# Kernel tuning notes

Hardware: AMD Instinct MI355X
Metric: run time of the kernel (lower is better)

Reference implementation:

```python
import jax, jax.numpy as jnp
import numpy as np

NEG_SLOPE = 0.2  # PyG GATv2Conv default negative_slope


def gatv2_conv(x, src, dst, n_nodes, Wl, bl, Wr, br, att, bias):
    """One GATv2Conv layer (concat=True, add_self_loops already applied).
    x: [N, Fin]; src/dst: [E]; Wl/Wr: [Fin, H*C]; att: [H, C]; bias: [H*C].
    Returns [N, H*C]."""
    H, C = att.shape
    xl = (x @ Wl + bl).reshape(n_nodes, H, C)  # source transform (x_j)
    xr = (x @ Wr + br).reshape(n_nodes, H, C)  # target transform (x_i)
    # per-edge GATv2 score: a^T LeakyReLU(xl_j + xr_i)
    e = jax.nn.leaky_relu(xl[src] + xr[dst], NEG_SLOPE)      # [E, H, C]
    score = jnp.einsum('ehc,hc->eh', e, att)                 # [E, H]
    # segment softmax over incoming edges of each destination node
    m = jax.lax.stop_gradient(
        jax.ops.segment_max(score, dst, num_segments=n_nodes))  # [N, H]
    p = jnp.exp(score - m[dst])                               # [E, H]
    s = jax.ops.segment_sum(p, dst, num_segments=n_nodes)     # [N, H]
    alpha = p / s[dst]                                        # [E, H]
    out = jax.ops.segment_sum(alpha[:, :, None] * xl[src], dst,
                              num_segments=n_nodes)           # [N, H, C]
    return out.reshape(n_nodes, H * C) + bias


def setup_inputs() -> dict:
    key = jax.random.key(0)
    ks = jax.random.split(key, 16)
    N, Fin, H, C = 20000, 64, 4, 64
    E = 500000
    Fmid = H * C  # 256

    def glorot(k, shape):
        fan_in, fan_out = shape[0], shape[-1]
        lim = np.sqrt(6.0 / (fan_in + fan_out))
        return jax.random.uniform(k, shape, jnp.float32, -lim, lim)

    return {
        'x': jax.random.normal(ks[0], (N, Fin), jnp.float32),
        'edge_index': jax.random.randint(ks[1], (2, E), 0, N, jnp.int64),
        # layer 1: in=64, out=64, heads=4
        'Wl1': glorot(ks[2], (Fin, H * C)),
        'bl1': jnp.zeros((H * C,), jnp.float32),
        'Wr1': glorot(ks[3], (Fin, H * C)),
        'br1': jnp.zeros((H * C,), jnp.float32),
        'att1': glorot(ks[4], (H, C)),
        'bias1': jnp.zeros((H * C,), jnp.float32),
        # layer 2: in=256, out=64, heads=4
        'Wl2': glorot(ks[5], (Fmid, H * C)),
        'bl2': jnp.zeros((H * C,), jnp.float32),
        'Wr2': glorot(ks[6], (Fmid, H * C)),
        'br2': jnp.zeros((H * C,), jnp.float32),
        'att2': glorot(ks[7], (H, C)),
        'bias2': jnp.zeros((H * C,), jnp.float32),
    }


def reference(x, edge_index, Wl1, bl1, Wr1, br1, att1, bias1,
              Wl2, bl2, Wr2, br2, att2, bias2):
    N = x.shape[0]
    # PyG add_self_loops=True default
    loop = jnp.arange(N, dtype=edge_index.dtype)
    src = jnp.concatenate([edge_index[0], loop])
    dst = jnp.concatenate([edge_index[1], loop])

    h = gatv2_conv(x, src, dst, N, Wl1, bl1, Wr1, br1, att1, bias1)
    h = jax.nn.elu(h)
    h = gatv2_conv(h, src, dst, N, Wl2, bl2, Wr2, br2, att2, bias2)
    return (h, jax.nn.log_softmax(h, axis=1))
```

## Files before the change

kernel.cpp:

```cpp
#include <hip/hip_runtime.h>
#include <math.h>

#define NEG_SLOPE 0.2f

typedef unsigned short ushort_t;
typedef __attribute__((ext_vector_type(8))) short short8;
typedef __attribute__((ext_vector_type(4))) float float4v;
typedef _Float16 half2v __attribute__((ext_vector_type(2)));

#if defined(__has_builtin)
#if __has_builtin(__builtin_amdgcn_fdot2)
#define HAS_FDOT2 1
#endif
#if __has_builtin(__builtin_amdgcn_update_dpp)
#define HAS_DPP 1
#endif
#endif

__device__ __forceinline__ ushort_t f2bf(float f) {
    unsigned u = __float_as_uint(f);
    return (ushort_t)((u + 0x7fffu + ((u >> 16) & 1u)) >> 16);
}
__device__ __forceinline__ unsigned pack2bf(float lo, float hi) {
    return ((unsigned)f2bf(hi) << 16) | (unsigned)f2bf(lo);
}

#if HAS_DPP
template <int CTRL>
__device__ __forceinline__ float dppf(float x) {
    return __uint_as_float((unsigned)__builtin_amdgcn_update_dpp(
        0, (int)__float_as_uint(x), CTRL, 0xF, 0xF, true));
}
#endif

__global__ void hist_kernel(const int* __restrict__ dst, int* __restrict__ deg, int E) {
    int i = blockIdx.x * 256 + threadIdx.x;
    if (i < E) atomicAdd(&deg[dst[i]], 1);
}

__global__ void partial_kernel(const int* __restrict__ deg, int* __restrict__ partial, int n) {
    const int t = threadIdx.x;
    const int i = blockIdx.x * 256 + t;
    int v = (i < n) ? deg[i] : 0;
#pragma unroll
    for (int off = 32; off > 0; off >>= 1) v += __shfl_xor(v, off, 64);
    __shared__ int ws[4];
    if ((t & 63) == 0) ws[t >> 6] = v;
    __syncthreads();
    if (t == 0) partial[blockIdx.x] = ws[0] + ws[1] + ws[2] + ws[3];
}

__global__ void scan_kernel(const int* __restrict__ in, int* __restrict__ out, int n) {
    __shared__ int sm[1024];
    __shared__ int carry_s;
    const int t = threadIdx.x;
    if (t == 0) { carry_s = 0; out[0] = 0; }
    __syncthreads();
    for (int base = 0; base < n; base += 1024) {
        int v = (base + t < n) ? in[base + t] : 0;
        sm[t] = v;
        __syncthreads();
        for (int off = 1; off < 1024; off <<= 1) {
            int u = (t >= off) ? sm[t - off] : 0;
            __syncthreads();
            sm[t] += u;
            __syncthreads();
        }
        if (base + t < n) out[base + t + 1] = carry_s + sm[t];
        __syncthreads();
        if (t == 0) carry_s += sm[1023];
        __syncthreads();
    }
}

__global__ void scan_block_kernel(const int* __restrict__ deg, const int* __restrict__ blk_off,
                                  int* __restrict__ row_ptr, int n) {
    const int t = threadIdx.x;
    const int i = blockIdx.x * 256 + t;
    const int lane = t & 63, w = t >> 6;
    int x = (i < n) ? deg[i] : 0;
#pragma unroll
    for (int off = 1; off < 64; off <<= 1) {
        int u = __shfl_up(x, off, 64);
        if (lane >= off) x += u;
    }
    __shared__ int ws[4];
    if (lane == 63) ws[w] = x;
    __syncthreads();
    int add = blk_off[blockIdx.x];
#pragma unroll
    for (int j = 0; j < 4; ++j)
        if (j < w) add += ws[j];
    if (i < n) row_ptr[i + 1] = add + x;
    if (i == 0) row_ptr[0] = 0;
}

__global__ void scatter_kernel(const int* __restrict__ src, const int* __restrict__ dst,
                               const int* __restrict__ row_ptr, int* __restrict__ cursor,
                               int* __restrict__ csr_src, int E) {
    int i = blockIdx.x * 256 + threadIdx.x;
    if (i < E) {
        int d = dst[i];
        int pos = row_ptr[d] + atomicAdd(&cursor[d], 1);
        csr_src[pos] = src[i];
    }
}

__global__ void wt_all_kernel(const float* __restrict__ W1l, const float* __restrict__ W1r,
                              const float* __restrict__ W2l, const float* __restrict__ W2r,
                              ushort_t* __restrict__ T1l, ushort_t* __restrict__ T1r,
                              ushort_t* __restrict__ T2l, ushort_t* __restrict__ T2r) {
    const int b = blockIdx.x;
    const float* W;
    ushort_t* T;
    int K, idx;
    if (b < 64)       { W = W1l; T = T1l; K = 64;  idx = b * 256 + threadIdx.x; }
    else if (b < 128) { W = W1r; T = T1r; K = 64;  idx = (b - 64) * 256 + threadIdx.x; }
    else if (b < 384) { W = W2l; T = T2l; K = 256; idx = (b - 128) * 256 + threadIdx.x; }
    else              { W = W2r; T = T2r; K = 256; idx = (b - 384) * 256 + threadIdx.x; }
    const int k = idx >> 8, c = idx & 255;
    T[(size_t)c * K + k] = f2bf(W[idx]);
}

template <int K, bool A_FP32>
__global__ __launch_bounds__(256) void gemm_dual_kernel(const void* __restrict__ Av,
                                                        const ushort_t* __restrict__ BTl,
                                                        const ushort_t* __restrict__ BTr,
                                                        const float* __restrict__ bl,
                                                        const float* __restrict__ br,
                                                        _Float16* __restrict__ outl,
                                                        _Float16* __restrict__ outr, int M) {
    __shared__ ushort_t As[2][64][40];
    __shared__ ushort_t Bs[2][2][128][40];
    const int t = threadIdx.x;
    const int row0 = blockIdx.x * 64, col0 = blockIdx.y * 128;
    const int wid = t >> 6, lane = t & 63;
    const int wr = wid >> 1, wc = wid & 1;
    const int frow = lane & 15, fk = (lane >> 4) * 8;
    const int arow = t >> 2, ak8 = (t & 3) * 8;
    const int srow = t >> 1, sks = (t & 1) * 16;

    float4v acc[2][2][4];
#pragma unroll
    for (int m = 0; m < 2; ++m)
#pragma unroll
        for (int i = 0; i < 2; ++i)
#pragma unroll
            for (int j = 0; j < 4; ++j) acc[m][i][j] = (float4v){0.f, 0.f, 0.f, 0.f};

    auto stage = [&](int buf, int k0) {
        uint4 va = make_uint4(0, 0, 0, 0);
        if (row0 + arow < M) {
            if (A_FP32) {
                const float* Xf = (const float*)Av + (size_t)(row0 + arow) * K + k0 + ak8;
                float4 x0 = *(const float4*)(Xf + 0);
                float4 x1 = *(const float4*)(Xf + 4);
                va = make_uint4(pack2bf(x0.x, x0.y), pack2bf(x0.z, x0.w),
                                pack2bf(x1.x, x1.y), pack2bf(x1.z, x1.w));
            } else {
                va = *(const uint4*)((const ushort_t*)Av + (size_t)(row0 + arow) * K + k0 + ak8);
            }
        }
        *(uint4*)&As[buf][arow][ak8] = va;
        const ushort_t* Bp = BTl + (size_t)(col0 + srow) * K + k0 + sks;
        *(uint4*)&Bs[buf][0][srow][sks + 0] = *(const uint4*)(Bp + 0);
        *(uint4*)&Bs[buf][0][srow][sks + 8] = *(const uint4*)(Bp + 8);
        const ushort_t* Bq = BTr + (size_t)(col0 + srow) * K + k0 + sks;
        *(uint4*)&Bs[buf][1][srow][sks + 0] = *(const uint4*)(Bq + 0);
        *(uint4*)&Bs[buf][1][srow][sks + 8] = *(const uint4*)(Bq + 8);
    };

    stage(0, 0);
    __syncthreads();
    int cur = 0;
    for (int k0 = 0; k0 < K; k0 += 32) {
        if (k0 + 32 < K) stage(cur ^ 1, k0 + 32);
        short8 af[2], bf[2][4];
#pragma unroll
        for (int mi = 0; mi < 2; ++mi)
            af[mi] = *(const short8*)&As[cur][wr * 32 + mi * 16 + frow][fk];
#pragma unroll
        for (int m = 0; m < 2; ++m)
#pragma unroll
            for (int ni = 0; ni < 4; ++ni)
                bf[m][ni] = *(const short8*)&Bs[cur][m][wc * 64 + ni * 16 + frow][fk];
#pragma unroll
        for (int m = 0; m < 2; ++m)
#pragma unroll
            for (int mi = 0; mi < 2; ++mi)
#pragma unroll
                for (int ni = 0; ni < 4; ++ni)
                    acc[m][mi][ni] = __builtin_amdgcn_mfma_f32_16x16x32_bf16(
                        af[mi], bf[m][ni], acc[m][mi][ni], 0, 0, 0);
        __syncthreads();
        cur ^= 1;
    }

    const int crow = (lane >> 4) * 4;
#pragma unroll
    for (int ni = 0; ni < 4; ++ni) {
        const int col = col0 + wc * 64 + ni * 16 + frow;
        const float bvl = bl[col], bvr = br[col];
#pragma unroll
        for (int mi = 0; mi < 2; ++mi) {
#pragma unroll
            for (int r = 0; r < 4; ++r) {
                const int row = row0 + wr * 32 + mi * 16 + crow + r;
                if (row < M) {
                    outl[(size_t)row * 256 + col] = (_Float16)(acc[0][mi][ni][r] + bvl);
                    outr[(size_t)row * 256 + col] = (_Float16)(acc[1][mi][ni][r] + bvr);
                }
            }
        }
    }
}

__global__ __launch_bounds__(128) void gat_fused_kernel(const int* __restrict__ csr_src,
                                                        const int* __restrict__ row_ptr,
                                                        const _Float16* __restrict__ xl,
                                                        const _Float16* __restrict__ xr,
                                                        const float* __restrict__ att,
                                                        const float* __restrict__ bias,
                                                        ushort_t* __restrict__ out_b,
                                                        float* __restrict__ out,
                                                        float* __restrict__ out_ls,
                                                        int n_nodes, int apply_elu) {
    const int wv = threadIdx.x >> 6;
    const int d = blockIdx.x * 2 + wv;
    if (d >= n_nodes) return;
    const int lane = threadIdx.x & 63;
    const int e = lane >> 5;
    const int g = lane & 31;
    const int off = g * 8;

    union U8 { uint4 u; _Float16 h[8]; half2v h2[4]; };
    U8 xru;
    xru.u = *(const uint4*)(xr + (size_t)d * 256 + off);
    float avf[8];
    *(float4*)&avf[0] = *(const float4*)(att + off);
    *(float4*)&avf[4] = *(const float4*)(att + off + 4);
#if HAS_FDOT2
    half2v xr2[4], a06[4], a04[4];
#pragma unroll
    for (int i = 0; i < 4; ++i) {
        xr2[i] = xru.h2[i];
        a06[i] = (half2v){(_Float16)(0.6f * avf[2 * i]), (_Float16)(0.6f * avf[2 * i + 1])};
        a04[i] = (half2v){(_Float16)(0.4f * avf[2 * i]), (_Float16)(0.4f * avf[2 * i + 1])};
    }
#else
    float xrf[8];
#pragma unroll
    for (int i = 0; i < 8; ++i) xrf[i] = (float)xru.h[i];
#endif
    const int e0 = row_ptr[d];
    const int deg = row_ptr[d + 1] - e0;
    const int cnt = deg + 1;
    const int nchunk = (cnt + 1) >> 1;
    float m = -INFINITY, s_loc = 0.f;
    float acc8[8] = {0.f, 0.f, 0.f, 0.f, 0.f, 0.f, 0.f, 0.f};

    U8 gc;
    {
        const int j = e;
        const int sn = (j < deg) ? csr_src[e0 + j] : d;
        gc.u = *(const uint4*)(xl + (size_t)sn * 256 + off);
    }
    int sn_nxt = d;
    if (nchunk > 1) {
        const int j = 2 + e;
        sn_nxt = (j < deg) ? csr_src[e0 + j] : d;
    }

    for (int c = 0; c < nchunk; ++c) {
        const int base = c << 1;
        int sn_n2 = d;
        if (c + 2 < nchunk) {
            const int j = base + 4 + e;
            sn_n2 = (j < deg) ? csr_src[e0 + j] : d;
        }
        U8 gn;
        gn.u = make_uint4(0, 0, 0, 0);
        if (c + 1 < nchunk) gn.u = *(const uint4*)(xl + (size_t)sn_nxt * 256 + off);

        const int j = base + e;
        float sc = 0.f;
#if HAS_FDOT2
#pragma unroll
        for (int i = 0; i < 4; ++i) {
            half2v v = gc.h2[i] + xr2[i];
            unsigned vb = __builtin_bit_cast(unsigned, v);
            half2v va = __builtin_bit_cast(half2v, vb & 0x7fff7fffu);
            sc = __builtin_amdgcn_fdot2(v, a06[i], sc, false);
            sc = __builtin_amdgcn_fdot2(va, a04[i], sc, false);
        }
#else
#pragma unroll
        for (int i = 0; i < 8; ++i) {
            float v = (float)gc.h[i] + xrf[i];
            v = fmaxf(v, NEG_SLOPE * v);
            sc = fmaf(v, avf[i], sc);
        }
#endif
#if HAS_DPP
        sc += dppf<0xB1>(sc);
        sc += dppf<0x4E>(sc);
#else
        sc += __shfl_xor(sc, 1, 64);
        sc += __shfl_xor(sc, 2, 64);
#endif
        sc += __shfl_xor(sc, 4, 64);
        sc = (j < cnt) ? sc : -INFINITY;
        float mx = fmaxf(sc, __shfl_xor(sc, 32, 64));
        if (mx > m + 8.f) {
            const float g2f = __expf(m - mx);
            s_loc *= g2f;
#pragma unroll
            for (int i = 0; i < 8; ++i) acc8[i] *= g2f;
            m = mx;
        }
        const float p = __expf(sc - m);
        s_loc += p;
#pragma unroll
        for (int i = 0; i < 8; ++i)
            acc8[i] = fmaf(p, (float)gc.h[i], acc8[i]);

        gc = gn;
        sn_nxt = sn_n2;
    }

    float s_tot = s_loc + __shfl_xor(s_loc, 32, 64);
#pragma unroll
    for (int i = 0; i < 8; ++i) acc8[i] += __shfl_xor(acc8[i], 32, 64);
    const float inv_s = 1.f / s_tot;
    float o8[8];
    const float* bp = bias + off;
#pragma unroll
    for (int i = 0; i < 8; ++i) o8[i] = acc8[i] * inv_s + bp[i];

    if (apply_elu) {
#pragma unroll
        for (int i = 0; i < 8; ++i) o8[i] = o8[i] > 0.f ? o8[i] : (__expf(o8[i]) - 1.f);
        if (e == 0) {
            uint4 u;
            u.x = pack2bf(o8[0], o8[1]);
            u.y = pack2bf(o8[2], o8[3]);
            u.z = pack2bf(o8[4], o8[5]);
            u.w = pack2bf(o8[6], o8[7]);
            *(uint4*)(out_b + (size_t)d * 256 + off) = u;
        }
    } else {
        if (e == 0) {
            float* op = out + (size_t)d * 256 + off;
            *(float4*)op       = make_float4(o8[0], o8[1], o8[2], o8[3]);
            *(float4*)(op + 4) = make_float4(o8[4], o8[5], o8[6], o8[7]);
        }
        float mx = o8[0];
#pragma unroll
        for (int i = 1; i < 8; ++i) mx = fmaxf(mx, o8[i]);
        mx = fmaxf(mx, __shfl_xor(mx, 1, 64));
        mx = fmaxf(mx, __shfl_xor(mx, 2, 64));
        mx = fmaxf(mx, __shfl_xor(mx, 4, 64));
        mx = fmaxf(mx, __shfl_xor(mx, 8, 64));
        mx = fmaxf(mx, __shfl_xor(mx, 16, 64));
        float se = 0.f;
#pragma unroll
        for (int i = 0; i < 8; ++i) se += __expf(o8[i] - mx);
        se += __shfl_xor(se, 1, 64);
        se += __shfl_xor(se, 2, 64);
        se += __shfl_xor(se, 4, 64);
        se += __shfl_xor(se, 8, 64);
        se += __shfl_xor(se, 16, 64);
        const float lg = mx + __logf(se);
        if (e == 0) {
            float* lp = out_ls + (size_t)d * 256 + off;
            *(float4*)lp       = make_float4(o8[0] - lg, o8[1] - lg, o8[2] - lg, o8[3] - lg);
            *(float4*)(lp + 4) = make_float4(o8[4] - lg, o8[5] - lg, o8[6] - lg, o8[7] - lg);
        }
    }
}

extern "C" void kernel_launch(void* const* d_in, const int* in_sizes, int n_in,
                              void* d_out, int out_size, void* d_ws, size_t ws_size,
                              hipStream_t stream) {
    const float* x     = (const float*)d_in[0];
    const int*   edge  = (const int*)d_in[1];
    const float* Wl1   = (const float*)d_in[2];
    const float* bl1   = (const float*)d_in[3];
    const float* Wr1   = (const float*)d_in[4];
    const float* br1   = (const float*)d_in[5];
    const float* att1  = (const float*)d_in[6];
    const float* bias1 = (const float*)d_in[7];
    const float* Wl2   = (const float*)d_in[8];
    const float* bl2   = (const float*)d_in[9];
    const float* Wr2   = (const float*)d_in[10];
    const float* br2   = (const float*)d_in[11];
    const float* att2  = (const float*)d_in[12];
    const float* bias2 = (const float*)d_in[13];

    const int N = in_sizes[0] / 64;
    const int E = in_sizes[1] / 2;
    const int* srcI = edge;
    const int* dstI = edge + E;

    const size_t NM = (size_t)N * 256;
    _Float16*  XR   = (_Float16*)d_ws;
    ushort_t*  XB   = (ushort_t*)(XR + NM);
    _Float16*  XL   = (_Float16*)(XB + NM);
    ushort_t*  WT1l = (ushort_t*)(XL + NM);
    ushort_t*  WT1r = WT1l + 256 * 64;
    ushort_t*  WT2l = WT1r + 256 * 64;
    ushort_t*  WT2r = WT2l + 256 * 256;
    int* deg     = (int*)(WT2r + 256 * 256);
    int* cursor  = deg + N;
    int* row_ptr = cursor + N;
    int* partial = row_ptr + N + 1;
    int* blk_off = partial + ((N + 255) / 256);
    int* csr_src = blk_off + ((N + 255) / 256) + 1;

    const int nb = (N + 255) / 256;
    const int e_grid = (E + 255) / 256;
    const dim3 gemm_grid((N + 63) / 64, 2);
    const int gat_grid = (N + 1) / 2;

    wt_all_kernel<<<640, 256, 0, stream>>>(Wl1, Wr1, Wl2, Wr2, WT1l, WT1r, WT2l, WT2r);

    hipMemsetAsync(deg, 0, (size_t)(2 * N) * sizeof(int), stream);
    hist_kernel<<<e_grid, 256, 0, stream>>>(dstI, deg, E);
    partial_kernel<<<nb, 256, 0, stream>>>(deg, partial, N);
    scan_kernel<<<1, 1024, 0, stream>>>(partial, blk_off, nb);
    scan_block_kernel<<<nb, 256, 0, stream>>>(deg, blk_off, row_ptr, N);
    scatter_kernel<<<e_grid, 256, 0, stream>>>(srcI, dstI, row_ptr, cursor, csr_src, E);

    gemm_dual_kernel<64, true><<<gemm_grid, 256, 0, stream>>>(x, WT1l, WT1r, bl1, br1,
                                                              XL, XR, N);
    gat_fused_kernel<<<gat_grid, 128, 0, stream>>>(csr_src, row_ptr, XL, XR, att1, bias1,
                                                   XB, nullptr, nullptr, N, 1);

    gemm_dual_kernel<256, false><<<gemm_grid, 256, 0, stream>>>(XB, WT2l, WT2r, bl2, br2,
                                                                XL, XR, N);
    float* h2 = (float*)d_out;
    gat_fused_kernel<<<gat_grid, 128, 0, stream>>>(csr_src, row_ptr, XL, XR, att2, bias2,
                                                   nullptr, h2, h2 + NM, N, 0);
}
```

Measured before the change: 200.6 us.

## Process four edges per wave step with 16 lanes per edge row

Remaps the fused attention/aggregation kernel so each wave handles four edges per iteration, with 16 lanes each covering 16 channels, instead of two edges with 32 lanes of 8 channels. Each head's 64 channels now span 4 lanes, so the head-score reduction needs one fewer shuffle, and the number of serial online-softmax steps per node is halved. Cost: more registers per lane (16 accumulators and two gather buffers), an extra cross-group max and a final reduce over four edge groups. Low-degree nodes also waste more lanes on padded edges.

```diff
diff --git a/kernel.cpp b/kernel.cpp
--- a/kernel.cpp
+++ b/kernel.cpp
@@ -229,76 +229,102 @@
     const int d = blockIdx.x * 2 + wv;
     if (d >= n_nodes) return;
     const int lane = threadIdx.x & 63;
-    const int e = lane >> 5;
-    const int g = lane & 31;
-    const int off = g * 8;
+    const int e = lane >> 4;
+    const int g = lane & 15;
+    const int off = g * 16;
 
     union U8 { uint4 u; _Float16 h[8]; half2v h2[4]; };
-    U8 xru;
-    xru.u = *(const uint4*)(xr + (size_t)d * 256 + off);
-    float avf[8];
-    *(float4*)&avf[0] = *(const float4*)(att + off);
-    *(float4*)&avf[4] = *(const float4*)(att + off + 4);
+    U8 xr0, xr1;
+    xr0.u = *(const uint4*)(xr + (size_t)d * 256 + off);
+    xr1.u = *(const uint4*)(xr + (size_t)d * 256 + off + 8);
+    float avf[16];
+#pragma unroll
+    for (int q = 0; q < 4; ++q)
+        *(float4*)&avf[q * 4] = *(const float4*)(att + off + q * 4);
 #if HAS_FDOT2
-    half2v xr2[4], a06[4], a04[4];
-#pragma unroll
-    for (int i = 0; i < 4; ++i) {
-        xr2[i] = xru.h2[i];
+    half2v xr2[8], a06[8], a04[8];
+#pragma unroll
+    for (int i = 0; i < 4; ++i) { xr2[i] = xr0.h2[i]; xr2[4 + i] = xr1.h2[i]; }
+#pragma unroll
+    for (int i = 0; i < 8; ++i) {
         a06[i] = (half2v){(_Float16)(0.6f * avf[2 * i]), (_Float16)(0.6f * avf[2 * i + 1])};
         a04[i] = (half2v){(_Float16)(0.4f * avf[2 * i]), (_Float16)(0.4f * avf[2 * i + 1])};
     }
 #else
-    float xrf[8];
-#pragma unroll
-    for (int i = 0; i < 8; ++i) xrf[i] = (float)xru.h[i];
+    float xrf[16];
+#pragma unroll
+    for (int i = 0; i < 8; ++i) { xrf[i] = (float)xr0.h[i]; xrf[8 + i] = (float)xr1.h[i]; }
 #endif
     const int e0 = row_ptr[d];
     const int deg = row_ptr[d + 1] - e0;
     const int cnt = deg + 1;
-    const int nchunk = (cnt + 1) >> 1;
+    const int nchunk = (cnt + 3) >> 2;
     float m = -INFINITY, s_loc = 0.f;
-    float acc8[8] = {0.f, 0.f, 0.f, 0.f, 0.f, 0.f, 0.f, 0.f};
-
-    U8 gc;
+    float acc[16];
+#pragma unroll
+    for (int i = 0; i < 16; ++i) acc[i] = 0.f;
+
+    U8 gc0, gc1;
     {
         const int j = e;
         const int sn = (j < deg) ? csr_src[e0 + j] : d;
-        gc.u = *(const uint4*)(xl + (size_t)sn * 256 + off);
+        const _Float16* p = xl + (size_t)sn * 256 + off;
+        gc0.u = *(const uint4*)p;
+        gc1.u = *(const uint4*)(p + 8);
     }
     int sn_nxt = d;
     if (nchunk > 1) {
-        const int j = 2 + e;
+        const int j = 4 + e;
         sn_nxt = (j < deg) ? csr_src[e0 + j] : d;
     }
 
     for (int c = 0; c < nchunk; ++c) {
-        const int base = c << 1;
+        const int base = c << 2;
         int sn_n2 = d;
         if (c + 2 < nchunk) {
-            const int j = base + 4 + e;
+            const int j = base + 8 + e;
             sn_n2 = (j < deg) ? csr_src[e0 + j] : d;
         }
-        U8 gn;
-        gn.u = make_uint4(0, 0, 0, 0);
-        if (c + 1 < nchunk) gn.u = *(const uint4*)(xl + (size_t)sn_nxt * 256 + off);
+        U8 gn0, gn1;
+        gn0.u = make_uint4(0, 0, 0, 0);
+        gn1.u = make_uint4(0, 0, 0, 0);
+        if (c + 1 < nchunk) {
+            const _Float16* p = xl + (size_t)sn_nxt * 256 + off;
+            gn0.u = *(const uint4*)p;
+            gn1.u = *(const uint4*)(p + 8);
+        }
 
         const int j = base + e;
         float sc = 0.f;
 #if HAS_FDOT2
 #pragma unroll
         for (int i = 0; i < 4; ++i) {
-            half2v v = gc.h2[i] + xr2[i];
+            half2v v = gc0.h2[i] + xr2[i];
             unsigned vb = __builtin_bit_cast(unsigned, v);
             half2v va = __builtin_bit_cast(half2v, vb & 0x7fff7fffu);
             sc = __builtin_amdgcn_fdot2(v, a06[i], sc, false);
             sc = __builtin_amdgcn_fdot2(va, a04[i], sc, false);
         }
+#pragma unroll
+        for (int i = 0; i < 4; ++i) {
+            half2v v = gc1.h2[i] + xr2[4 + i];
+            unsigned vb = __builtin_bit_cast(unsigned, v);
+            half2v va = __builtin_bit_cast(half2v, vb & 0x7fff7fffu);
+            sc = __builtin_amdgcn_fdot2(v, a06[4 + i], sc, false);
+            sc = __builtin_amdgcn_fdot2(va, a04[4 + i], sc, false);
+        }
 #else
 #pragma unroll
         for (int i = 0; i < 8; ++i) {
-            float v = (float)gc.h[i] + xrf[i];
+            float v = (float)gc0.h[i] + xrf[i];
             v = fmaxf(v, NEG_SLOPE * v);
             sc = fmaf(v, avf[i], sc);
+        }
+#pragma unroll
+        for (int i = 0; i < 8; ++i) {
+            float v = (float)gc1.h[i] + xrf[8 + i];
+            v = fmaxf(v, NEG_SLOPE * v);
+            sc = fmaf(v, avf[8 + i], sc);
         }
 #endif
 #if HAS_DPP
@@ -308,73 +334,89 @@
         sc += __shfl_xor(sc, 1, 64);
         sc += __shfl_xor(sc, 2, 64);
 #endif
-        sc += __shfl_xor(sc, 4, 64);
         sc = (j < cnt) ? sc : -INFINITY;
-        float mx = fmaxf(sc, __shfl_xor(sc, 32, 64));
+        float mx = fmaxf(sc, __shfl_xor(sc, 16, 64));
+        mx = fmaxf(mx, __shfl_xor(mx, 32, 64));
         if (mx > m + 8.f) {
             const float g2f = __expf(m - mx);
             s_loc *= g2f;
 #pragma unroll
-            for (int i = 0; i < 8; ++i) acc8[i] *= g2f;
+            for (int i = 0; i < 16; ++i) acc[i] *= g2f;
             m = mx;
         }
         const float p = __expf(sc - m);
         s_loc += p;
 #pragma unroll
         for (int i = 0; i < 8; ++i)
-            acc8[i] = fmaf(p, (float)gc.h[i], acc8[i]);
-
-        gc = gn;
+            acc[i] = fmaf(p, (float)gc0.h[i], acc[i]);
+#pragma unroll
+        for (int i = 0; i < 8; ++i)
+            acc[8 + i] = fmaf(p, (float)gc1.h[i], acc[8 + i]);
+
+        gc0 = gn0;
+        gc1 = gn1;
         sn_nxt = sn_n2;
     }
 
-    float s_tot = s_loc + __shfl_xor(s_loc, 32, 64);
-#pragma unroll
-    for (int i = 0; i < 8; ++i) acc8[i] += __shfl_xor(acc8[i], 32, 64);
+    float s_tot = s_loc + __shfl_xor(s_loc, 16, 64);
+    s_tot += __shfl_xor(s_tot, 32, 64);
+#pragma unroll
+    for (int i = 0; i < 16; ++i) {
+        acc[i] += __shfl_xor(acc[i], 16, 64);
+        acc[i] += __shfl_xor(acc[i], 32, 64);
+    }
     const float inv_s = 1.f / s_tot;
-    float o8[8];
+    float o[16];
     const float* bp = bias + off;
 #pragma unroll
-    for (int i = 0; i < 8; ++i) o8[i] = acc8[i] * inv_s + bp[i];
+    for (int i = 0; i < 16; ++i) o[i] = acc[i] * inv_s + bp[i];
 
     if (apply_elu) {
 #pragma unroll
-        for (int i = 0; i < 8; ++i) o8[i] = o8[i] > 0.f ? o8[i] : (__expf(o8[i]) - 1.f);
+        for (int i = 0; i < 16; ++i) o[i] = o[i] > 0.f ? o[i] : (__expf(o[i]) - 1.f);
         if (e == 0) {
-            uint4 u;
-            u.x = pack2bf(o8[0], o8[1]);
-            u.y = pack2bf(o8[2], o8[3]);
-            u.z = pack2bf(o8[4], o8[5]);
-            u.w = pack2bf(o8[6], o8[7]);
-            *(uint4*)(out_b + (size_t)d * 256 + off) = u;
+            uint4 u0, u1;
+            u0.x = pack2bf(o[0], o[1]);
+            u0.y = pack2bf(o[2], o[3]);
+            u0.z = pack2bf(o[4], o[5]);
+            u0.w = pack2bf(o[6], o[7]);
+            u1.x = pack2bf(o[8], o[9]);
+            u1.y = pack2bf(o[10], o[11]);
+            u1.z = pack2bf(o[12], o[13]);
+            u1.w = pack2bf(o[14], o[15]);
+            ushort_t* op = out_b + (size_t)d * 256 + off;
+            *(uint4*)op       = u0;
+            *(uint4*)(op + 8) = u1;
         }
     } else {
         if (e == 0) {
             float* op = out + (size_t)d * 256 + off;
-            *(float4*)op       = make_float4(o8[0], o8[1], o8[2], o8[3]);
-            *(float4*)(op + 4) = make_float4(o8[4], o8[5], o8[6], o8[7]);
-        }
-        float mx = o8[0];
-#pragma unroll
-        for (int i = 1; i < 8; ++i) mx = fmaxf(mx, o8[i]);
+#pragma unroll
+            for (int q = 0; q < 4; ++q)
+                *(float4*)(op + q * 4) = make_float4(o[q * 4], o[q * 4 + 1],
+                                                     o[q * 4 + 2], o[q * 4 + 3]);
+        }
+        float mx = o[0];
+#pragma unroll
+        for (int i = 1; i < 16; ++i) mx = fmaxf(mx, o[i]);
         mx = fmaxf(mx, __shfl_xor(mx, 1, 64));
         mx = fmaxf(mx, __shfl_xor(mx, 2, 64));
         mx = fmaxf(mx, __shfl_xor(mx, 4, 64));
         mx = fmaxf(mx, __shfl_xor(mx, 8, 64));
-        mx = fmaxf(mx, __shfl_xor(mx, 16, 64));
         float se = 0.f;
 #pragma unroll
-        for (int i = 0; i < 8; ++i) se += __expf(o8[i] - mx);
+        for (int i = 0; i < 16; ++i) se += __expf(o[i] - mx);
         se += __shfl_xor(se, 1, 64);
         se += __shfl_xor(se, 2, 64);
         se += __shfl_xor(se, 4, 64);
         se += __shfl_xor(se, 8, 64);
-        se += __shfl_xor(se, 16, 64);
         const float lg = mx + __logf(se);
         if (e == 0) {
             float* lp = out_ls + (size_t)d * 256 + off;
-            *(float4*)lp       = make_float4(o8[0] - lg, o8[1] - lg, o8[2] - lg, o8[3] - lg);
-            *(float4*)(lp + 4) = make_float4(o8[4] - lg, o8[5] - lg, o8[6] - lg, o8[7] - lg);
+#pragma unroll
+            for (int q = 0; q < 4; ++q)
+                *(float4*)(lp + q * 4) = make_float4(o[q * 4] - lg, o[q * 4 + 1] - lg,
+                                                     o[q * 4 + 2] - lg, o[q * 4 + 3] - lg);
         }
     }
 }
```

After: 197.0 us. About the same (-1.8%).

## Switch to head-major feature layout with per-head GAT kernels and separate log-softmax

Applied to the files above, without the earlier changes.

The GEMM now writes xl/xr in a head-major layout ([H][N][64]). Aggregation runs as four per-head kernel launches, so each gathered source row is 128 bytes and the per-head working set (about 2.5MB fp16) fits in cache. A wave now processes 8 edges per chunk, one 64-channel head each, instead of 2 edges across all 256 channels. Log-softmax moves into its own kernel, and the CSR scatter reuses the per-edge rank returned by the histogram atomics instead of a second atomic pass. The cost is extra launches, an extra read and write of the output for log-softmax, and wider shuffle reductions.

```diff
diff --git a/kernel.cpp b/kernel.cpp
--- a/kernel.cpp
+++ b/kernel.cpp
@@ -33,9 +33,10 @@
 }
 #endif
 
-__global__ void hist_kernel(const int* __restrict__ dst, int* __restrict__ deg, int E) {
+__global__ void hist_kernel(const int* __restrict__ dst, int* __restrict__ deg,
+                            int* __restrict__ rank, int E) {
     int i = blockIdx.x * 256 + threadIdx.x;
-    if (i < E) atomicAdd(&deg[dst[i]], 1);
+    if (i < E) rank[i] = atomicAdd(&deg[dst[i]], 1);
 }
 
 __global__ void partial_kernel(const int* __restrict__ deg, int* __restrict__ partial, int n) {
@@ -96,13 +97,12 @@
 }
 
 __global__ void scatter_kernel(const int* __restrict__ src, const int* __restrict__ dst,
-                               const int* __restrict__ row_ptr, int* __restrict__ cursor,
+                               const int* __restrict__ row_ptr, const int* __restrict__ rank,
                                int* __restrict__ csr_src, int E) {
     int i = blockIdx.x * 256 + threadIdx.x;
     if (i < E) {
         int d = dst[i];
-        int pos = row_ptr[d] + atomicAdd(&cursor[d], 1);
-        csr_src[pos] = src[i];
+        csr_src[row_ptr[d] + rank[i]] = src[i];
     }
 }
 
@@ -201,44 +201,44 @@
     for (int ni = 0; ni < 4; ++ni) {
         const int col = col0 + wc * 64 + ni * 16 + frow;
         const float bvl = bl[col], bvr = br[col];
+        const size_t hbase = (size_t)(col >> 6) * M * 64 + (col & 63);
 #pragma unroll
         for (int mi = 0; mi < 2; ++mi) {
 #pragma unroll
             for (int r = 0; r < 4; ++r) {
                 const int row = row0 + wr * 32 + mi * 16 + crow + r;
                 if (row < M) {
-                    outl[(size_t)row * 256 + col] = (_Float16)(acc[0][mi][ni][r] + bvl);
-                    outr[(size_t)row * 256 + col] = (_Float16)(acc[1][mi][ni][r] + bvr);
+                    outl[hbase + (size_t)row * 64] = (_Float16)(acc[0][mi][ni][r] + bvl);
+                    outr[hbase + (size_t)row * 64] = (_Float16)(acc[1][mi][ni][r] + bvr);
                 }
             }
         }
     }
 }
 
-__global__ __launch_bounds__(128) void gat_fused_kernel(const int* __restrict__ csr_src,
-                                                        const int* __restrict__ row_ptr,
-                                                        const _Float16* __restrict__ xl,
-                                                        const _Float16* __restrict__ xr,
-                                                        const float* __restrict__ att,
-                                                        const float* __restrict__ bias,
-                                                        ushort_t* __restrict__ out_b,
-                                                        float* __restrict__ out,
-                                                        float* __restrict__ out_ls,
-                                                        int n_nodes, int apply_elu) {
+__global__ __launch_bounds__(128) void gat_head_kernel(const int* __restrict__ csr_src,
+                                                       const int* __restrict__ row_ptr,
+                                                       const _Float16* __restrict__ xlh,
+                                                       const _Float16* __restrict__ xrh,
+                                                       const float* __restrict__ atth,
+                                                       const float* __restrict__ biash,
+                                                       ushort_t* __restrict__ outb,
+                                                       float* __restrict__ outf,
+                                                       int n_nodes, int apply_elu) {
     const int wv = threadIdx.x >> 6;
     const int d = blockIdx.x * 2 + wv;
     if (d >= n_nodes) return;
     const int lane = threadIdx.x & 63;
-    const int e = lane >> 5;
-    const int g = lane & 31;
+    const int e = lane >> 3;
+    const int g = lane & 7;
     const int off = g * 8;
 
     union U8 { uint4 u; _Float16 h[8]; half2v h2[4]; };
     U8 xru;
-    xru.u = *(const uint4*)(xr + (size_t)d * 256 + off);
+    xru.u = *(const uint4*)(xrh + (size_t)d * 64 + off);
     float avf[8];
-    *(float4*)&avf[0] = *(const float4*)(att + off);
-    *(float4*)&avf[4] = *(const float4*)(att + off + 4);
+    *(float4*)&avf[0] = *(const float4*)(atth + off);
+    *(float4*)&avf[4] = *(const float4*)(atth + off + 4);
 #if HAS_FDOT2
     half2v xr2[4], a06[4], a04[4];
 #pragma unroll
@@ -255,32 +255,32 @@
     const int e0 = row_ptr[d];
     const int deg = row_ptr[d + 1] - e0;
     const int cnt = deg + 1;
-    const int nchunk = (cnt + 1) >> 1;
+    const int nchunk = (cnt + 7) >> 3;
     float m = -INFINITY, s_loc = 0.f;
-    float acc8[8] = {0.f, 0.f, 0.f, 0.f, 0.f, 0.f, 0.f, 0.f};
+    float acc[8] = {0.f, 0.f, 0.f, 0.f, 0.f, 0.f, 0.f, 0.f};
 
     U8 gc;
     {
         const int j = e;
         const int sn = (j < deg) ? csr_src[e0 + j] : d;
-        gc.u = *(const uint4*)(xl + (size_t)sn * 256 + off);
+        gc.u = *(const uint4*)(xlh + (size_t)sn * 64 + off);
     }
     int sn_nxt = d;
     if (nchunk > 1) {
-        const int j = 2 + e;
+        const int j = 8 + e;
         sn_nxt = (j < deg) ? csr_src[e0 + j] : d;
     }
 
     for (int c = 0; c < nchunk; ++c) {
-        const int base = c << 1;
+        const int base = c << 3;
         int sn_n2 = d;
         if (c + 2 < nchunk) {
-            const int j = base + 4 + e;
+            const int j = base + 16 + e;
             sn_n2 = (j < deg) ? csr_src[e0 + j] : d;
         }
         U8 gn;
         gn.u = make_uint4(0, 0, 0, 0);
-        if (c + 1 < nchunk) gn.u = *(const uint4*)(xl + (size_t)sn_nxt * 256 + off);
+        if (c + 1 < nchunk) gn.u = *(const uint4*)(xlh + (size_t)sn_nxt * 64 + off);
 
         const int j = base + e;
         float sc = 0.f;
@@ -310,73 +310,80 @@
 #endif
         sc += __shfl_xor(sc, 4, 64);
         sc = (j < cnt) ? sc : -INFINITY;
-        float mx = fmaxf(sc, __shfl_xor(sc, 32, 64));
+        float mx = fmaxf(sc, __shfl_xor(sc, 8, 64));
+        mx = fmaxf(mx, __shfl_xor(mx, 16, 64));
+        mx = fmaxf(mx, __shfl_xor(mx, 32, 64));
         if (mx > m + 8.f) {
             const float g2f = __expf(m - mx);
             s_loc *= g2f;
 #pragma unroll
-            for (int i = 0; i < 8; ++i) acc8[i] *= g2f;
+            for (int i = 0; i < 8; ++i) acc[i] *= g2f;
             m = mx;
         }
         const float p = __expf(sc - m);
         s_loc += p;
 #pragma unroll
         for (int i = 0; i < 8; ++i)
-            acc8[i] = fmaf(p, (float)gc.h[i], acc8[i]);
+            acc[i] = fmaf(p, (float)gc.h[i], acc[i]);
 
         gc = gn;
         sn_nxt = sn_n2;
     }
 
-    float s_tot = s_loc + __shfl_xor(s_loc, 32, 64);
-#pragma unroll
-    for (int i = 0; i < 8; ++i) acc8[i] += __shfl_xor(acc8[i], 32, 64);
+    float s_tot = s_loc + __shfl_xor(s_loc, 8, 64);
+    s_tot += __shfl_xor(s_tot, 16, 64);
+    s_tot += __shfl_xor(s_tot, 32, 64);
+#pragma unroll
+    for (int i = 0; i < 8; ++i) {
+        acc[i] += __shfl_xor(acc[i], 8, 64);
+        acc[i] += __shfl_xor(acc[i], 16, 64);
+        acc[i] += __shfl_xor(acc[i], 32, 64);
+    }
     const float inv_s = 1.f / s_tot;
-    float o8[8];
-    const float* bp = bias + off;
-#pragma unroll
-    for (int i = 0; i < 8; ++i) o8[i] = acc8[i] * inv_s + bp[i];
+    float o[8];
+#pragma unroll
+    for (int i = 0; i < 8; ++i) o[i] = acc[i] * inv_s + biash[off + i];
 
     if (apply_elu) {
 #pragma unroll
-        for (int i = 0; i < 8; ++i) o8[i] = o8[i] > 0.f ? o8[i] : (__expf(o8[i]) - 1.f);
+        for (int i = 0; i < 8; ++i) o[i] = o[i] > 0.f ? o[i] : (__expf(o[i]) - 1.f);
         if (e == 0) {
             uint4 u;
-            u.x = pack2bf(o8[0], o8[1]);
-            u.y = pack2bf(o8[2], o8[3]);
-            u.z = pack2bf(o8[4], o8[5]);
-            u.w = pack2bf(o8[6], o8[7]);
-            *(uint4*)(out_b + (size_t)d * 256 + off) = u;
+            u.x = pack2bf(o[0], o[1]);
+            u.y = pack2bf(o[2], o[3]);
+            u.z = pack2bf(o[4], o[5]);
+            u.w = pack2bf(o[6], o[7]);
+            *(uint4*)(outb + (size_t)d * 256 + off) = u;
         }
     } else {
         if (e == 0) {
-            float* op = out + (size_t)d * 256 + off;
-            *(float4*)op       = make_float4(o8[0], o8[1], o8[2], o8[3]);
-            *(float4*)(op + 4) = make_float4(o8[4], o8[5], o8[6], o8[7]);
-        }
-        float mx = o8[0];
-#pragma unroll
-        for (int i = 1; i < 8; ++i) mx = fmaxf(mx, o8[i]);
-        mx = fmaxf(mx, __shfl_xor(mx, 1, 64));
-        mx = fmaxf(mx, __shfl_xor(mx, 2, 64));
-        mx = fmaxf(mx, __shfl_xor(mx, 4, 64));
-        mx = fmaxf(mx, __shfl_xor(mx, 8, 64));
-        mx = fmaxf(mx, __shfl_xor(mx, 16, 64));
-        float se = 0.f;
-#pragma unroll
-        for (int i = 0; i < 8; ++i) se += __expf(o8[i] - mx);
-        se += __shfl_xor(se, 1, 64);
-        se += __shfl_xor(se, 2, 64);
-        se += __shfl_xor(se, 4, 64);
-        se += __shfl_xor(se, 8, 64);
-        se += __shfl_xor(se, 16, 64);
-        const float lg = mx + __logf(se);
-        if (e == 0) {
-            float* lp = out_ls + (size_t)d * 256 + off;
-            *(float4*)lp       = make_float4(o8[0] - lg, o8[1] - lg, o8[2] - lg, o8[3] - lg);
-            *(float4*)(lp + 4) = make_float4(o8[4] - lg, o8[5] - lg, o8[6] - lg, o8[7] - lg);
-        }
-    }
+            float* op = outf + (size_t)d * 256 + off;
+            *(float4*)op       = make_float4(o[0], o[1], o[2], o[3]);
+            *(float4*)(op + 4) = make_float4(o[4], o[5], o[6], o[7]);
+        }
+    }
+}
+
+__global__ void log_softmax_kernel(const float* __restrict__ in,
+                                   float* __restrict__ out, int n_nodes) {
+    __shared__ float red[8];
+    const int n = blockIdx.x;
+    const int t = threadIdx.x;
+    const int wave = t >> 6, lane = t & 63;
+    const float v = in[(size_t)n * 256 + t];
+    float mx = v;
+#pragma unroll
+    for (int off = 32; off > 0; off >>= 1) mx = fmaxf(mx, __shfl_xor(mx, off, 64));
+    if (lane == 0) red[wave] = mx;
+    __syncthreads();
+    const float m4 = fmaxf(fmaxf(red[0], red[1]), fmaxf(red[2], red[3]));
+    float sum = __expf(v - m4);
+#pragma unroll
+    for (int off = 32; off > 0; off >>= 1) sum += __shfl_xor(sum, off, 64);
+    if (lane == 0) red[4 + wave] = sum;
+    __syncthreads();
+    const float s4 = (red[4] + red[5]) + (red[6] + red[7]);
+    out[(size_t)n * 256 + t] = v - m4 - __logf(s4);
 }
 
 extern "C" void kernel_launch(void* const* d_in, const int* in_sizes, int n_in,
@@ -403,6 +410,7 @@
     const int* dstI = edge + E;
 
     const size_t NM = (size_t)N * 256;
+    const size_t NH = (size_t)N * 64;
     _Float16*  XR   = (_Float16*)d_ws;
     ushort_t*  XB   = (ushort_t*)(XR + NM);
     _Float16*  XL   = (_Float16*)(XB + NM);
@@ -411,11 +419,11 @@
     ushort_t*  WT2l = WT1r + 256 * 64;
     ushort_t*  WT2r = WT2l + 256 * 256;
     int* deg     = (int*)(WT2r + 256 * 256);
-    int* cursor  = deg + N;
-    int* row_ptr = cursor + N;
+    int* row_ptr = deg + N;
     int* partial = row_ptr + N + 1;
     int* blk_off = partial + ((N + 255) / 256);
-    int* csr_src = blk_off + ((N + 255) / 256) + 1;
+    int* rank    = blk_off + ((N + 255) / 256) + 1;
+    int* csr_src = rank + E;
 
     const int nb = (N + 255) / 256;
     const int e_grid = (E + 255) / 256;
@@ -424,21 +432,28 @@
 
     wt_all_kernel<<<640, 256, 0, stream>>>(Wl1, Wr1, Wl2, Wr2, WT1l, WT1r, WT2l, WT2r);
 
-    hipMemsetAsync(deg, 0, (size_t)(2 * N) * sizeof(int), stream);
-    hist_kernel<<<e_grid, 256, 0, stream>>>(dstI, deg, E);
+    hipMemsetAsync(deg, 0, (size_t)N * sizeof(int), stream);
+    hist_kernel<<<e_grid, 256, 0, stream>>>(dstI, deg, rank, E);
     partial_kernel<<<nb, 256, 0, stream>>>(deg, partial, N);
     scan_kernel<<<1, 1024, 0, stream>>>(partial, blk_off, nb);
     scan_block_kernel<<<nb, 256, 0, stream>>>(deg, blk_off, row_ptr, N);
-    scatter_kernel<<<e_grid, 256, 0, stream>>>(srcI, dstI, row_ptr, cursor, csr_src, E);
+    scatter_kernel<<<e_grid, 256, 0, stream>>>(srcI, dstI, row_ptr, rank, csr_src, E);
 
     gemm_dual_kernel<64, true><<<gemm_grid, 256, 0, stream>>>(x, WT1l, WT1r, bl1, br1,
                                                               XL, XR, N);
-    gat_fused_kernel<<<gat_grid, 128, 0, stream>>>(csr_src, row_ptr, XL, XR, att1, bias1,
-                                                   XB, nullptr, nullptr, N, 1);
+    for (int h = 0; h < 4; ++h)
+        gat_head_kernel<<<gat_grid, 128, 0, stream>>>(csr_src, row_ptr,
+                                                      XL + (size_t)h * NH, XR + (size_t)h * NH,
+                                                      att1 + h * 64, bias1 + h * 64,
+                                                      XB + h * 64, nullptr, N, 1);
 
     gemm_dual_kernel<256, false><<<gemm_grid, 256, 0, stream>>>(XB, WT2l, WT2r, bl2, br2,
                                                                 XL, XR, N);
     float* h2 = (float*)d_out;
-    gat_fused_kernel<<<gat_grid, 128, 0, stream>>>(csr_src, row_ptr, XL, XR, att2, bias2,
-                                                   nullptr, h2, h2 + NM, N, 0);
-}
+    for (int h = 0; h < 4; ++h)
+        gat_head_kernel<<<gat_grid, 128, 0, stream>>>(csr_src, row_ptr,
+                                                      XL + (size_t)h * NH, XR + (size_t)h * NH,
+                                                      att2 + h * 64, bias2 + h * 64,
+                                                      nullptr, h2 + h * 64, N, 0);
+    log_softmax_kernel<<<N, 256, 0, stream>>>(h2, h2 + NM, N);
+}
```

New measurement: 245.3 us. 22.3% more time.
